# Performance work log

Measured on AMD Instinct MI355X. Metric: run time of the kernel, lower is better.

## Reference

```python
import jax, jax.numpy as jnp
import numpy as np
from jax import lax

IN_CH, OUT_CH, KS, GROUPS = 64, 64, 3, 8
FPG = IN_CH // GROUPS  # features per group = 8
PAD = KS // 2


def setup_inputs() -> dict:
    key = jax.random.key(0)
    k1, k2, k3 = jax.random.split(key, 3)
    x = jax.random.normal(k1, (8, IN_CH, 256, 256), dtype=jnp.float32)
    representation = jax.random.normal(k2, (8, 32), dtype=jnp.float32)
    # Linear(32, OUT_CH*KS*KS, bias=False) weight, torch layout (out_features, in_features)
    W = jax.random.normal(k3, (OUT_CH * KS * KS, 32), dtype=jnp.float32) * (1.0 / np.sqrt(32))
    return {"x": x, "representation": representation, "W": W}


def reference(x, representation, W):
    b = x.shape[0]
    # ReflectionPad2d
    xp = jnp.pad(x, ((0, 0), (0, 0), (PAD, PAD), (PAD, PAD)), mode="reflect")
    # compress_key: Linear (no bias) + LeakyReLU(0.1)
    k = jax.nn.leaky_relu(representation @ W.T, 0.1)  # [b, OUT_CH*KS*KS]
    kernel = k.reshape(b, OUT_CH, 1, KS, KS)
    # repeat_interleave on a size-1 dim == broadcast/tile
    kernel = jnp.broadcast_to(kernel, (b, OUT_CH, FPG, KS, KS))
    # per-sample grouped conv (equivalent to torch's batch-as-groups trick)
    def conv_one(xi, ki):
        # xi: [C,H,W], ki: [OUT_CH, FPG, KS, KS]
        out = lax.conv_general_dilated(
            xi[None], ki, window_strides=(1, 1), padding="VALID",
            dimension_numbers=("NCHW", "OIHW", "NCHW"),
            feature_group_count=GROUPS)
        return out[0]
    return jax.vmap(conv_one)(xp, kernel)  # [b, OUT_CH, H, W]
```

## Files before the change

kernel.cpp:

```cpp
#include <hip/hip_runtime.h>


#define LROW 260
#define TH 8

__device__ __forceinline__ int reflect1(int i, int n) {
  if (i < 0) i = -i;
  if (i >= n) i = 2 * n - 2 - i;
  return i;
}

__global__ __launch_bounds__(256) void dynconv_rows(
    const float* __restrict__ x,
    const float* __restrict__ rep,
    const float* __restrict__ W,
    float* __restrict__ out) {
  const int tid = threadIdx.x;
  const int ty = blockIdx.x & 31;
  const int g  = (blockIdx.x >> 5) & 7;
  const int b  = blockIdx.x >> 8;

  __shared__ float s[(TH + 2) * LROW];
  __shared__ float wl[96];

  if (tid < 72) {
    const int oc  = tid / 9;
    const int tap = tid - oc * 9;
    const int row = g * 72 + tid;
    const float* wr = W + (size_t)row * 32;
    const float* rb = rep + b * 32;
    float acc = 0.f;
#pragma unroll
    for (int j = 0; j < 32; ++j) acc += rb[j] * wr[j];
    wl[oc * 12 + tap] = (acc > 0.f) ? acc : 0.1f * acc;
  }

  const int gy0 = ty * TH;
  const float* xg = x + ((size_t)(b * 64 + g * 8)) * 65536;
  const float4* xg4 = (const float4*)xg;

#pragma unroll
  for (int it = 0; it < 3; ++it) {
    const int t = tid + it * 256;
    if (it < 2 || t < 640) {
      const int row = t >> 6, seg = t & 63;
      const int yy = reflect1(gy0 + row - 1, 256);
      const float4* p = xg4 + (size_t)yy * 64 + seg;
      float4 v0 = p[0 * 16384], v1 = p[1 * 16384], v2 = p[2 * 16384], v3 = p[3 * 16384];
      float4 v4 = p[4 * 16384], v5 = p[5 * 16384], v6 = p[6 * 16384], v7 = p[7 * 16384];
      float4 a;
      a.x = ((v0.x + v1.x) + (v2.x + v3.x)) + ((v4.x + v5.x) + (v6.x + v7.x));
      a.y = ((v0.y + v1.y) + (v2.y + v3.y)) + ((v4.y + v5.y) + (v6.y + v7.y));
      a.z = ((v0.z + v1.z) + (v2.z + v3.z)) + ((v4.z + v5.z) + (v6.z + v7.z));
      a.w = ((v0.w + v1.w) + (v2.w + v3.w)) + ((v4.w + v5.w) + (v6.w + v7.w));
      *(float4*)&s[row * LROW + seg * 4] = a;
    }
  }
  __syncthreads();

  const int cs = (tid & 63) * 4;
  const int r0 = tid >> 6;

#pragma unroll
  for (int it = 0; it < 2; ++it) {
    const int rr = r0 + it * 4;
    float win[3][6];
#pragma unroll
    for (int dy = 0; dy < 3; ++dy) {
      const float* row = &s[(rr + dy) * LROW];
      float4 a = *(const float4*)&row[cs];
      float  r = row[(cs == 252) ? 254 : cs + 4];
      float  l = row[(cs == 0) ? 1 : cs - 1];
      win[dy][0] = l;   win[dy][1] = a.x; win[dy][2] = a.y;
      win[dy][3] = a.z; win[dy][4] = a.w; win[dy][5] = r;
    }

    const int y = gy0 + rr;
    float* ob = out + (((size_t)(b * 64 + g * 8) * 256 + y) * 256 + cs);

#pragma unroll
    for (int oc = 0; oc < 8; ++oc) {
      const float* w = &wl[oc * 12];
      const float w00 = w[0], w01 = w[1], w02 = w[2];
      const float w10 = w[3], w11 = w[4], w12 = w[5];
      const float w20 = w[6], w21 = w[7], w22 = w[8];
      float4 o;
      o.x = w00 * win[0][0] + w01 * win[0][1] + w02 * win[0][2]
          + w10 * win[1][0] + w11 * win[1][1] + w12 * win[1][2]
          + w20 * win[2][0] + w21 * win[2][1] + w22 * win[2][2];
      o.y = w00 * win[0][1] + w01 * win[0][2] + w02 * win[0][3]
          + w10 * win[1][1] + w11 * win[1][2] + w12 * win[1][3]
          + w20 * win[2][1] + w21 * win[2][2] + w22 * win[2][3];
      o.z = w00 * win[0][2] + w01 * win[0][3] + w02 * win[0][4]
          + w10 * win[1][2] + w11 * win[1][3] + w12 * win[1][4]
          + w20 * win[2][2] + w21 * win[2][3] + w22 * win[2][4];
      o.w = w00 * win[0][3] + w01 * win[0][4] + w02 * win[0][5]
          + w10 * win[1][3] + w11 * win[1][4] + w12 * win[1][5]
          + w20 * win[2][3] + w21 * win[2][4] + w22 * win[2][5];
      *(float4*)(ob + (size_t)oc * 65536) = o;
    }
  }
}

extern "C" void kernel_launch(void* const* d_in, const int* in_sizes, int n_in,
                              void* d_out, int out_size, void* d_ws, size_t ws_size,
                              hipStream_t stream) {
  const float* x   = (const float*)d_in[0];
  const float* rep = (const float*)d_in[1];
  const float* W   = (const float*)d_in[2];
  float* out = (float*)d_out;
  hipLaunchKernelGGL(dynconv_rows, dim3(2048), dim3(256), 0, stream,
                     x, rep, W, out);
}
```

Baseline: 241.1 us.

## Split into group-sum pass to workspace and separate conv pass

Splits the fused kernel into two launches. The first sums the 8 input channels of each group into a workspace plane. The second reads that plane from global memory, applies the 3x3 dynamic kernel, and writes 8 output channels, one row per wave. This removes the recomputed halo rows of the tiled fused kernel and the shared-memory staging. In exchange it adds an extra write and read of a 16MB intermediate plus a second launch. The fused kernel is kept as a fallback when the workspace is too small.

```diff
diff --git a/kernel.cpp b/kernel.cpp
--- a/kernel.cpp
+++ b/kernel.cpp
@@ -1,8 +1,5 @@
 #include <hip/hip_runtime.h>
 
-
-#define LROW 260
-#define TH 8
 
 __device__ __forceinline__ int reflect1(int i, int n) {
   if (i < 0) i = -i;
@@ -10,17 +7,35 @@
   return i;
 }
 
-__global__ __launch_bounds__(256) void dynconv_rows(
+__global__ __launch_bounds__(256) void gsum_kernel(
     const float* __restrict__ x,
+    float* __restrict__ S) {
+  const int i = blockIdx.x * 256 + threadIdx.x;
+  const int plane = i >> 14;
+  const int off = i & 16383;
+  const float4* p = (const float4*)x + (size_t)plane * 8 * 16384 + off;
+  float4 a;
+  {
+    float4 v0 = p[0],         v1 = p[16384],     v2 = p[2 * 16384], v3 = p[3 * 16384];
+    float4 v4 = p[4 * 16384], v5 = p[5 * 16384], v6 = p[6 * 16384], v7 = p[7 * 16384];
+    a.x = ((v0.x + v1.x) + (v2.x + v3.x)) + ((v4.x + v5.x) + (v6.x + v7.x));
+    a.y = ((v0.y + v1.y) + (v2.y + v3.y)) + ((v4.y + v5.y) + (v6.y + v7.y));
+    a.z = ((v0.z + v1.z) + (v2.z + v3.z)) + ((v4.z + v5.z) + (v6.z + v7.z));
+    a.w = ((v0.w + v1.w) + (v2.w + v3.w)) + ((v4.w + v5.w) + (v6.w + v7.w));
+  }
+  ((float4*)S)[i] = a;
+}
+
+__global__ __launch_bounds__(256) void conv_rows(
+    const float* __restrict__ S,
     const float* __restrict__ rep,
     const float* __restrict__ W,
     float* __restrict__ out) {
   const int tid = threadIdx.x;
-  const int ty = blockIdx.x & 31;
-  const int g  = (blockIdx.x >> 5) & 7;
-  const int b  = blockIdx.x >> 8;
-
-  __shared__ float s[(TH + 2) * LROW];
+  const int rt = blockIdx.x & 63;
+  const int g  = (blockIdx.x >> 6) & 7;
+  const int b  = blockIdx.x >> 9;
+
   __shared__ float wl[96];
 
   if (tid < 72) {
@@ -34,8 +49,82 @@
     for (int j = 0; j < 32; ++j) acc += rb[j] * wr[j];
     wl[oc * 12 + tap] = (acc > 0.f) ? acc : 0.1f * acc;
   }
-
-  const int gy0 = ty * TH;
+  __syncthreads();
+
+  const int lane = tid & 63;
+  const int wv   = tid >> 6;
+  const int y    = rt * 4 + wv;
+  const int cs   = lane * 4;
+
+  const float* Sp = S + (size_t)(b * 8 + g) * 65536;
+  const int ym = reflect1(y - 1, 256);
+  const int yp = reflect1(y + 1, 256);
+  const int cl = (cs == 0) ? 1 : cs - 1;
+  const int cr = (cs == 252) ? 254 : cs + 4;
+
+  float win[3][6];
+  {
+    const int rows[3] = {ym, y, yp};
+#pragma unroll
+    for (int dy = 0; dy < 3; ++dy) {
+      const float* r = Sp + (size_t)rows[dy] * 256;
+      float4 a = *(const float4*)(r + cs);
+      win[dy][0] = r[cl]; win[dy][1] = a.x; win[dy][2] = a.y;
+      win[dy][3] = a.z;   win[dy][4] = a.w; win[dy][5] = r[cr];
+    }
+  }
+
+  float* ob = out + (((size_t)(b * 64 + g * 8) * 256 + y) * 256 + cs);
+
+#pragma unroll
+  for (int oc = 0; oc < 8; ++oc) {
+    const float* w = &wl[oc * 12];
+    const float w00 = w[0], w01 = w[1], w02 = w[2];
+    const float w10 = w[3], w11 = w[4], w12 = w[5];
+    const float w20 = w[6], w21 = w[7], w22 = w[8];
+    float4 o;
+    o.x = w00 * win[0][0] + w01 * win[0][1] + w02 * win[0][2]
+        + w10 * win[1][0] + w11 * win[1][1] + w12 * win[1][2]
+        + w20 * win[2][0] + w21 * win[2][1] + w22 * win[2][2];
+    o.y = w00 * win[0][1] + w01 * win[0][2] + w02 * win[0][3]
+        + w10 * win[1][1] + w11 * win[1][2] + w12 * win[1][3]
+        + w20 * win[2][1] + w21 * win[2][2] + w22 * win[2][3];
+    o.z = w00 * win[0][2] + w01 * win[0][3] + w02 * win[0][4]
+        + w10 * win[1][2] + w11 * win[1][3] + w12 * win[1][4]
+        + w20 * win[2][2] + w21 * win[2][3] + w22 * win[2][4];
+    o.w = w00 * win[0][3] + w01 * win[0][4] + w02 * win[0][5]
+        + w10 * win[1][3] + w11 * win[1][4] + w12 * win[1][5]
+        + w20 * win[2][3] + w21 * win[2][4] + w22 * win[2][5];
+    *(float4*)(ob + (size_t)oc * 65536) = o;
+  }
+}
+
+#define LROW 260
+#define FTH 8
+__global__ __launch_bounds__(256) void dynconv_rows(
+    const float* __restrict__ x, const float* __restrict__ rep,
+    const float* __restrict__ W, float* __restrict__ out) {
+  const int tid = threadIdx.x;
+  const int ty = blockIdx.x & 31;
+  const int g  = (blockIdx.x >> 5) & 7;
+  const int b  = blockIdx.x >> 8;
+
+  __shared__ float s[(FTH + 2) * LROW];
+  __shared__ float wl[96];
+
+  if (tid < 72) {
+    const int oc  = tid / 9;
+    const int tap = tid - oc * 9;
+    const int row = g * 72 + tid;
+    const float* wr = W + (size_t)row * 32;
+    const float* rb = rep + b * 32;
+    float acc = 0.f;
+#pragma unroll
+    for (int j = 0; j < 32; ++j) acc += rb[j] * wr[j];
+    wl[oc * 12 + tap] = (acc > 0.f) ? acc : 0.1f * acc;
+  }
+
+  const int gy0 = ty * FTH;
   const float* xg = x + ((size_t)(b * 64 + g * 8)) * 65536;
   const float4* xg4 = (const float4*)xg;
 
@@ -74,10 +163,8 @@
       win[dy][0] = l;   win[dy][1] = a.x; win[dy][2] = a.y;
       win[dy][3] = a.z; win[dy][4] = a.w; win[dy][5] = r;
     }
-
     const int y = gy0 + rr;
     float* ob = out + (((size_t)(b * 64 + g * 8) * 256 + y) * 256 + cs);
-
 #pragma unroll
     for (int oc = 0; oc < 8; ++oc) {
       const float* w = &wl[oc * 12];
@@ -109,6 +196,15 @@
   const float* rep = (const float*)d_in[1];
   const float* W   = (const float*)d_in[2];
   float* out = (float*)d_out;
-  hipLaunchKernelGGL(dynconv_rows, dim3(2048), dim3(256), 0, stream,
-                     x, rep, W, out);
-}
+
+  const size_t s_bytes = (size_t)8 * 8 * 256 * 256 * sizeof(float);
+  if (ws_size >= s_bytes) {
+    float* S = (float*)d_ws;
+    hipLaunchKernelGGL(gsum_kernel, dim3(4096), dim3(256), 0, stream, x, S);
+    hipLaunchKernelGGL(conv_rows, dim3(4096), dim3(256), 0, stream,
+                       S, rep, W, out);
+  } else {
+    hipLaunchKernelGGL(dynconv_rows, dim3(2048), dim3(256), 0, stream,
+                       x, rep, W, out);
+  }
+}
```

Result: no change. 240.1 us, median of 2 (-0.4%).
